# Kernel optimization log

Measured on AMD Instinct MI355X. Metric: run time of the kernel, lower is better.

The kernel has to match this reference:

```python
import jax, jax.numpy as jnp
import numpy as np

K_NODES = 4096
SEQ_L = 32
D_MODEL = 128
D_FF = 512
N_EDGES = 65536
LN_EPS = 1e-5
NEG_SLOPE = 0.2  # PyG GATConv default leaky_relu slope


def setup_inputs() -> dict:
    key = jax.random.key(0)
    ks = jax.random.split(key, 12)
    s = 0.02
    D, F = D_MODEL, D_FF
    return {
        "x": jax.random.normal(ks[0], (1, K_NODES, SEQ_L, D), jnp.float32),
        "edge_index": jax.random.randint(ks[1], (1, 2, N_EDGES), 0, K_NODES, dtype=jnp.int64),
        # temporal TransformerEncoderLayer params (norm_first, 1 head, gelu)
        "ln1_g": jnp.ones((D,), jnp.float32), "ln1_b": jnp.zeros((D,), jnp.float32),
        "qkv_w": jax.random.normal(ks[2], (3 * D, D), jnp.float32) * s,
        "qkv_b": jnp.zeros((3 * D,), jnp.float32),
        "out_w": jax.random.normal(ks[3], (D, D), jnp.float32) * s,
        "out_b": jnp.zeros((D,), jnp.float32),
        "ln2_g": jnp.ones((D,), jnp.float32), "ln2_b": jnp.zeros((D,), jnp.float32),
        "ff1_w": jax.random.normal(ks[4], (F, D), jnp.float32) * s,
        "ff1_b": jnp.zeros((F,), jnp.float32),
        "ff2_w": jax.random.normal(ks[5], (D, F), jnp.float32) * s,
        "ff2_b": jnp.zeros((D,), jnp.float32),
        # GATConv params (heads=1, concat -> out dim D)
        "gat_w": jax.random.normal(ks[6], (D, D), jnp.float32) * s,
        "att_src": jax.random.normal(ks[7], (D,), jnp.float32) * s,
        "att_dst": jax.random.normal(ks[8], (D,), jnp.float32) * s,
        "gat_b": jnp.zeros((D,), jnp.float32),
    }


def _ln(x, g, b):
    m = x.mean(-1, keepdims=True)
    v = ((x - m) ** 2).mean(-1, keepdims=True)
    return (x - m) * jax.lax.rsqrt(v + LN_EPS) * g + b


def _temporal(x, ln1_g, ln1_b, qkv_w, qkv_b, out_w, out_b, ln2_g, ln2_b,
              ff1_w, ff1_b, ff2_w, ff2_b):
    # x: [N, L, D]; pre-norm single-head self-attention + GELU FFN
    D = x.shape[-1]
    h = _ln(x, ln1_g, ln1_b)
    qkv = h @ qkv_w.T + qkv_b
    q, k, v = jnp.split(qkv, 3, axis=-1)
    scores = jnp.einsum('nqd,nkd->nqk', q, k) / jnp.sqrt(jnp.asarray(D, x.dtype))
    a = jax.nn.softmax(scores, axis=-1)
    attn = jnp.einsum('nqk,nkd->nqd', a, v) @ out_w.T + out_b
    x = x + attn
    h = _ln(x, ln2_g, ln2_b)
    ff = jax.nn.gelu(h @ ff1_w.T + ff1_b, approximate=False) @ ff2_w.T + ff2_b
    return x + ff


def _gat(x0, src, dst, gat_w, att_src, att_dst, gat_b):
    # x0: [K, L, D]; vectorized over L (replaces the per-timestep python loop)
    K = x0.shape[0]
    h = jnp.einsum('kld,ed->kle', x0, gat_w)              # [K, L, D]
    a_s = jnp.einsum('kld,d->kl', h, att_src)             # [K, L]
    a_d = jnp.einsum('kld,d->kl', h, att_dst)
    e = jax.nn.leaky_relu(a_s[src] + a_d[dst], NEG_SLOPE)  # [E', L]
    m = jax.ops.segment_max(e, dst, num_segments=K)
    ex = jnp.exp(e - m[dst])
    denom = jax.ops.segment_sum(ex, dst, num_segments=K)
    alpha = ex / (denom[dst] + 1e-16)
    out = jax.ops.segment_sum(h[src] * alpha[..., None], dst, num_segments=K)
    return out + gat_b


def reference(x, edge_index, ln1_g, ln1_b, qkv_w, qkv_b, out_w, out_b,
              ln2_g, ln2_b, ff1_w, ff1_b, ff2_w, ff2_b,
              gat_w, att_src, att_dst, gat_b):
    B, K, L, D = x.shape
    xt = _temporal(x.reshape(B * K, L, D), ln1_g, ln1_b, qkv_w, qkv_b,
                   out_w, out_b, ln2_g, ln2_b, ff1_w, ff1_b, ff2_w, ff2_b)
    xt = xt.reshape(B, K, L, D)
    # GATConv adds self-loops by default
    loops = jnp.arange(K, dtype=edge_index.dtype)
    src = jnp.concatenate([edge_index[0, 0], loops])
    dst = jnp.concatenate([edge_index[0, 1], loops])
    out0 = _gat(xt[0], src, dst, gat_w, att_src, att_dst, gat_b)  # [K, L, D]
    res = jnp.zeros_like(x).at[0].set(out0)
    return res
```

## Files before the change

### kernel.cpp

```cpp
#include <hip/hip_runtime.h>

#define KNODES 4096
#define SEQL 32
#define DM 128
#define DFF 512
#define NEDGE 65536
#define NETOT (NEDGE + KNODES)

typedef float f32x4 __attribute__((ext_vector_type(4)));
typedef short s16x8 __attribute__((ext_vector_type(8)));
typedef short s16x4 __attribute__((ext_vector_type(4)));

#define MFMA16(a, b, c) __builtin_amdgcn_mfma_f32_16x16x32_bf16(a, b, c, 0, 0, 0)

#define F_OUT 96
#define F_FF1 128
#define F_FF2 256
#define F_GAT 384
#define NFRAG 416

__device__ __forceinline__ short f2bf(float f) {
  union { float f; unsigned u; } v; v.f = f;
  unsigned r = (v.u + 0x7FFFu + ((v.u >> 16) & 1u)) >> 16;
  return (short)r;
}

__device__ __forceinline__ float gelu_exact(float v) {
  return 0.5f * v * (1.f + erff(v * 0.70710678118654752440f));
}

__device__ __forceinline__ void ln_to_bf16(const float* XF, short* AB,
                                           const float* __restrict__ g,
                                           const float* __restrict__ b,
                                           int r, int cb) {
  const float* xr = XF + r * 132 + cb;
  float v[8]; float s = 0.f, ss = 0.f;
#pragma unroll
  for (int i = 0; i < 8; ++i) { v[i] = xr[i]; s += v[i]; ss += v[i] * v[i]; }
  s += __shfl_xor(s, 1); ss += __shfl_xor(ss, 1);
  s += __shfl_xor(s, 2); ss += __shfl_xor(ss, 2);
  s += __shfl_xor(s, 4); ss += __shfl_xor(ss, 4);
  s += __shfl_xor(s, 8); ss += __shfl_xor(ss, 8);
  const float mean = s * (1.f / 128.f);
  const float var = ss * (1.f / 128.f) - mean * mean;
  const float rs = rsqrtf(var + 1e-5f);
  const float* gp = g + cb; const float* bp = b + cb;
  short o[8];
#pragma unroll
  for (int i = 0; i < 8; ++i) o[i] = f2bf((v[i] - mean) * rs * gp[i] + bp[i]);
  *(s16x8*)(AB + r * 136 + cb) = *(s16x8*)o;
}

__global__ __launch_bounds__(512, 4) void temporal_kernel(
    const float* __restrict__ x,
    const float* __restrict__ ln1_g, const float* __restrict__ ln1_b,
    const short* __restrict__ wpk, const float* __restrict__ qkv_b,
    const float* __restrict__ out_b,
    const float* __restrict__ ln2_g, const float* __restrict__ ln2_b,
    const float* __restrict__ ff1_b, const float* __restrict__ ff2_b,
    const float* __restrict__ att_src, const float* __restrict__ att_dst,
    short* __restrict__ h_out, float* __restrict__ as_out, float* __restrict__ ad_out) {
  __shared__ __align__(16) char smem[53248];
  float* XF = (float*)smem;
  short* AB = (short*)(smem + 16896);
  float* Sf = (float*)(smem + 16896);
  short* Pb = (short*)(smem + 21504);
  short* Qb = (short*)(smem + 25600);
  short* Kb = (short*)(smem + 34304);
  short* Fb = (short*)(smem + 25600);
  short* Vt = (short*)(smem + 43008);

  const int t = threadIdx.x;
  const int w = t >> 6;
  const int lane = t & 63;
  const int q = lane >> 4, c = lane & 15;
  const int n = blockIdx.x;
  const int r16 = t >> 4, cb8 = (t & 15) * 8;

#define WPK(f) ((const s16x8*)(wpk + (size_t)(f) * 512 + lane * 8))

  s16x8 bwq[3][4];
#pragma unroll
  for (int ii = 0; ii < 3; ++ii)
#pragma unroll
    for (int kt = 0; kt < 4; ++kt)
      bwq[ii][kt] = *WPK((w * 3 + ii) * 4 + kt);

  {
#pragma unroll
    for (int i = t; i < 1024; i += 512) {
      const int row = i >> 5, c4i = i & 31;
      *(float4*)(XF + row * 132 + c4i * 4) =
          *(const float4*)(x + (size_t)n * (SEQL * DM) + i * 4);
    }
  }
  __syncthreads();

  ln_to_bf16(XF, AB, ln1_g, ln1_b, r16, cb8);
  __syncthreads();

  {
    s16x8 a[2][4];
#pragma unroll
    for (int mt = 0; mt < 2; ++mt)
#pragma unroll
      for (int kt = 0; kt < 4; ++kt)
        a[mt][kt] = *(const s16x8*)(AB + (mt * 16 + c) * 136 + kt * 32 + q * 8);
#pragma unroll
    for (int ii = 0; ii < 3; ++ii) {
      const int n0 = (w * 3 + ii) * 16;
      f32x4 acc0 = {0.f, 0.f, 0.f, 0.f}, acc1 = {0.f, 0.f, 0.f, 0.f};
#pragma unroll
      for (int kt = 0; kt < 4; ++kt) {
        acc0 = MFMA16(a[0][kt], bwq[ii][kt], acc0);
        acc1 = MFMA16(a[1][kt], bwq[ii][kt], acc1);
      }
      const float bias = qkv_b[n0 + c];
      if (n0 < 128) {
#pragma unroll
        for (int i = 0; i < 4; ++i) {
          Qb[(q * 4 + i) * 136 + n0 + c] = f2bf(acc0[i] + bias);
          Qb[(16 + q * 4 + i) * 136 + n0 + c] = f2bf(acc1[i] + bias);
        }
      } else if (n0 < 256) {
        const int cc = n0 - 128 + c;
#pragma unroll
        for (int i = 0; i < 4; ++i) {
          Kb[(q * 4 + i) * 136 + cc] = f2bf(acc0[i] + bias);
          Kb[(16 + q * 4 + i) * 136 + cc] = f2bf(acc1[i] + bias);
        }
      } else {
        const int d = n0 - 256 + c;
        s16x4 p0, p1;
#pragma unroll
        for (int i = 0; i < 4; ++i) { p0[i] = f2bf(acc0[i] + bias); p1[i] = f2bf(acc1[i] + bias); }
        *(s16x4*)(Vt + d * 40 + q * 4) = p0;
        *(s16x4*)(Vt + d * 40 + 16 + q * 4) = p1;
      }
    }
  }
  __syncthreads();

  if (w < 4) {
    const int mt = w & 1, nt = w >> 1;
    s16x8 aq[4], bk[4];
#pragma unroll
    for (int kt = 0; kt < 4; ++kt) {
      aq[kt] = *(const s16x8*)(Qb + (mt * 16 + c) * 136 + kt * 32 + q * 8);
      bk[kt] = *(const s16x8*)(Kb + (nt * 16 + c) * 136 + kt * 32 + q * 8);
    }
    f32x4 acc = {0.f, 0.f, 0.f, 0.f};
#pragma unroll
    for (int kt = 0; kt < 4; ++kt) acc = MFMA16(aq[kt], bk[kt], acc);
#pragma unroll
    for (int i = 0; i < 4; ++i)
      Sf[(mt * 16 + q * 4 + i) * 36 + nt * 16 + c] = acc[i] * 0.08838834764831845f;
  }
  __syncthreads();

  if (t < 256) {
    const int r8 = t >> 3, c4 = (t & 7) * 4;
    float4 sv = *(const float4*)(Sf + r8 * 36 + c4);
    float mx = fmaxf(fmaxf(sv.x, sv.y), fmaxf(sv.z, sv.w));
    mx = fmaxf(mx, __shfl_xor(mx, 1));
    mx = fmaxf(mx, __shfl_xor(mx, 2));
    mx = fmaxf(mx, __shfl_xor(mx, 4));
    float e0 = expf(sv.x - mx), e1 = expf(sv.y - mx), e2 = expf(sv.z - mx), e3 = expf(sv.w - mx);
    float sum = e0 + e1 + e2 + e3;
    sum += __shfl_xor(sum, 1);
    sum += __shfl_xor(sum, 2);
    sum += __shfl_xor(sum, 4);
    const float inv = 1.f / sum;
    s16x4 pw; pw[0] = f2bf(e0 * inv); pw[1] = f2bf(e1 * inv); pw[2] = f2bf(e2 * inv); pw[3] = f2bf(e3 * inv);
    *(s16x4*)(Pb + r8 * 40 + c4) = pw;
  }
  __syncthreads();

  s16x8 bwp[4];
  {
#pragma unroll
    for (int kt = 0; kt < 4; ++kt) bwp[kt] = *WPK(F_OUT + w * 4 + kt);
    s16x8 ap0 = *(const s16x8*)(Pb + c * 40 + q * 8);
    s16x8 ap1 = *(const s16x8*)(Pb + (16 + c) * 40 + q * 8);
    const int d0 = w * 16;
    s16x8 bv = *(const s16x8*)(Vt + (d0 + c) * 40 + q * 8);
    f32x4 acc0 = {0.f, 0.f, 0.f, 0.f}, acc1 = {0.f, 0.f, 0.f, 0.f};
    acc0 = MFMA16(ap0, bv, acc0);
    acc1 = MFMA16(ap1, bv, acc1);
#pragma unroll
    for (int i = 0; i < 4; ++i) {
      Qb[(q * 4 + i) * 136 + d0 + c] = f2bf(acc0[i]);
      Qb[(16 + q * 4 + i) * 136 + d0 + c] = f2bf(acc1[i]);
    }
  }
  __syncthreads();

  {
    s16x8 aa[2][4];
#pragma unroll
    for (int mt = 0; mt < 2; ++mt)
#pragma unroll
      for (int kt = 0; kt < 4; ++kt)
        aa[mt][kt] = *(const s16x8*)(Qb + (mt * 16 + c) * 136 + kt * 32 + q * 8);
    const int n0 = w * 16;
    f32x4 acc0 = {0.f, 0.f, 0.f, 0.f}, acc1 = {0.f, 0.f, 0.f, 0.f};
#pragma unroll
    for (int kt = 0; kt < 4; ++kt) {
      acc0 = MFMA16(aa[0][kt], bwp[kt], acc0);
      acc1 = MFMA16(aa[1][kt], bwp[kt], acc1);
    }
    const float bias = out_b[n0 + c];
#pragma unroll
    for (int i = 0; i < 4; ++i) {
      XF[(q * 4 + i) * 132 + n0 + c] += acc0[i] + bias;
      XF[(16 + q * 4 + i) * 132 + n0 + c] += acc1[i] + bias;
    }
  }
  __syncthreads();

  ln_to_bf16(XF, AB, ln2_g, ln2_b, r16, cb8);
  __syncthreads();

  {
    s16x8 af[2][4];
#pragma unroll
    for (int mt = 0; mt < 2; ++mt)
#pragma unroll
      for (int kt = 0; kt < 4; ++kt)
        af[mt][kt] = *(const s16x8*)(AB + (mt * 16 + c) * 136 + kt * 32 + q * 8);
    f32x4 facc0 = {0.f, 0.f, 0.f, 0.f}, facc1 = {0.f, 0.f, 0.f, 0.f};

    for (int ch = 0; ch < 2; ++ch) {
      s16x8 bw1[2][4], bw2[8];
#pragma unroll
      for (int ii = 0; ii < 2; ++ii)
#pragma unroll
        for (int kt = 0; kt < 4; ++kt)
          bw1[ii][kt] = *WPK(F_FF1 + (ch * 16 + w * 2 + ii) * 4 + kt);
#pragma unroll
      for (int kt = 0; kt < 8; ++kt)
        bw2[kt] = *WPK(F_FF2 + w * 16 + ch * 8 + kt);

#pragma unroll
      for (int ii = 0; ii < 2; ++ii) {
        const int ntl = w * 2 + ii;
        const int n0g = ch * 256 + ntl * 16;
        f32x4 acc0 = {0.f, 0.f, 0.f, 0.f}, acc1 = {0.f, 0.f, 0.f, 0.f};
#pragma unroll
        for (int kt = 0; kt < 4; ++kt) {
          acc0 = MFMA16(af[0][kt], bw1[ii][kt], acc0);
          acc1 = MFMA16(af[1][kt], bw1[ii][kt], acc1);
        }
        const float bias = ff1_b[n0g + c];
#pragma unroll
        for (int i = 0; i < 4; ++i) {
          Fb[(q * 4 + i) * 264 + ntl * 16 + c] = f2bf(gelu_exact(acc0[i] + bias));
          Fb[(16 + q * 4 + i) * 264 + ntl * 16 + c] = f2bf(gelu_exact(acc1[i] + bias));
        }
      }
      __syncthreads();
#pragma unroll
      for (int kt = 0; kt < 8; ++kt) {
        s16x8 a0 = *(const s16x8*)(Fb + c * 264 + kt * 32 + q * 8);
        s16x8 a1 = *(const s16x8*)(Fb + (16 + c) * 264 + kt * 32 + q * 8);
        facc0 = MFMA16(a0, bw2[kt], facc0);
        facc1 = MFMA16(a1, bw2[kt], facc1);
      }
      __syncthreads();
    }
    {
      const int n0 = w * 16;
      const float bias = ff2_b[n0 + c];
#pragma unroll
      for (int i = 0; i < 4; ++i) {
        const int r0 = q * 4 + i, r1 = 16 + q * 4 + i;
        AB[r0 * 136 + n0 + c] = f2bf(XF[r0 * 132 + n0 + c] + facc0[i] + bias);
        AB[r1 * 136 + n0 + c] = f2bf(XF[r1 * 132 + n0 + c] + facc1[i] + bias);
      }
    }
  }
  s16x8 bwg[4];
#pragma unroll
  for (int kt = 0; kt < 4; ++kt) bwg[kt] = *WPK(F_GAT + w * 4 + kt);
  __syncthreads();

  {
    s16x8 ag[2][4];
#pragma unroll
    for (int mt = 0; mt < 2; ++mt)
#pragma unroll
      for (int kt = 0; kt < 4; ++kt)
        ag[mt][kt] = *(const s16x8*)(AB + (mt * 16 + c) * 136 + kt * 32 + q * 8);
    const int n0 = w * 16;
    f32x4 acc0 = {0.f, 0.f, 0.f, 0.f}, acc1 = {0.f, 0.f, 0.f, 0.f};
#pragma unroll
    for (int kt = 0; kt < 4; ++kt) {
      acc0 = MFMA16(ag[0][kt], bwg[kt], acc0);
      acc1 = MFMA16(ag[1][kt], bwg[kt], acc1);
    }
#pragma unroll
    for (int i = 0; i < 4; ++i) {
      const int r0 = q * 4 + i, r1 = 16 + q * 4 + i;
      XF[r0 * 132 + n0 + c] = acc0[i];
      XF[r1 * 132 + n0 + c] = acc1[i];
    }
  }
  __syncthreads();

  {
    const int row = t >> 4;
    const float* xr = XF + row * 132 + cb8;
    short o[8];
#pragma unroll
    for (int i = 0; i < 8; ++i) o[i] = f2bf(xr[i]);
    *(s16x8*)(h_out + ((size_t)n * SEQL + row) * DM + cb8) = *(s16x8*)o;
  }

  if (t < 64) {
    const int row = t & 31;
    const float* vec = (t < 32) ? att_src : att_dst;
    const float* hr = XF + row * 132;
    float s = 0.f;
#pragma unroll
    for (int d = 0; d < DM; d += 4)
      s += hr[d] * vec[d] + hr[d + 1] * vec[d + 1] + hr[d + 2] * vec[d + 2] + hr[d + 3] * vec[d + 3];
    if (t < 32) as_out[n * SEQL + row] = s;
    else        ad_out[n * SEQL + row] = s;
  }
}

__global__ void cvt_weights(const float* __restrict__ qkv_w, const float* __restrict__ out_w,
                            const float* __restrict__ ff1_w, const float* __restrict__ ff2_w,
                            const float* __restrict__ gat_w, short* __restrict__ wpk) {
  const int u = blockIdx.x * 256 + threadIdx.x;
  if (u >= NFRAG * 64) return;
  const int f = u >> 6, lane = u & 63;
  const int q = lane >> 4, c = lane & 15;
  const float* src; int row, kt, ld;
  if (f < F_OUT)       { src = qkv_w; ld = 128; int g = f;         row = (g >> 2) * 16 + c; kt = g & 3; }
  else if (f < F_FF1)  { src = out_w; ld = 128; int g = f - F_OUT; row = (g >> 2) * 16 + c; kt = g & 3; }
  else if (f < F_FF2)  { src = ff1_w; ld = 128; int g = f - F_FF1; row = (g >> 2) * 16 + c; kt = g & 3; }
  else if (f < F_GAT)  { src = ff2_w; ld = 512; int g = f - F_FF2; row = (g >> 4) * 16 + c; kt = g & 15; }
  else                 { src = gat_w; ld = 128; int g = f - F_GAT; row = (g >> 2) * 16 + c; kt = g & 3; }
  const float* p = src + row * ld + kt * 32 + q * 8;
  const float4 v0 = *(const float4*)p;
  const float4 v1 = *(const float4*)(p + 4);
  s16x8 o;
  o[0] = f2bf(v0.x); o[1] = f2bf(v0.y); o[2] = f2bf(v0.z); o[3] = f2bf(v0.w);
  o[4] = f2bf(v1.x); o[5] = f2bf(v1.y); o[6] = f2bf(v1.z); o[7] = f2bf(v1.w);
  *(s16x8*)(wpk + (size_t)f * 512 + lane * 8) = o;
}

__global__ void zero_counts(int* counts) {
  int i = blockIdx.x * 256 + threadIdx.x;
  if (i < KNODES) counts[i] = 0;
}

__global__ void hist_kernel(const int* __restrict__ ei, int* counts) {
  int i = blockIdx.x * 256 + threadIdx.x;
  if (i < NETOT) {
    int dst = (i < NEDGE) ? ei[NEDGE + i] : (i - NEDGE);
    atomicAdd(&counts[dst], 1);
  }
}

__global__ void scan_kernel(const int* __restrict__ counts, int* offs, int* cursor) {
  __shared__ int tmp[1024];
  const int t = threadIdx.x;
  const int base = t * 4;
  int c0 = counts[base], c1 = counts[base + 1], c2 = counts[base + 2], c3 = counts[base + 3];
  const int s = c0 + c1 + c2 + c3;
  tmp[t] = s;
  __syncthreads();
  for (int off = 1; off < 1024; off <<= 1) {
    int v = (t >= off) ? tmp[t - off] : 0;
    __syncthreads();
    tmp[t] += v;
    __syncthreads();
  }
  int o = tmp[t] - s;
  offs[base] = o; cursor[base] = o; o += c0;
  offs[base + 1] = o; cursor[base + 1] = o; o += c1;
  offs[base + 2] = o; cursor[base + 2] = o; o += c2;
  offs[base + 3] = o; cursor[base + 3] = o; o += c3;
  if (t == 1023) offs[KNODES] = o;
}

__global__ void scatter_kernel(const int* __restrict__ ei, int* cursor, int* __restrict__ csr) {
  int i = blockIdx.x * 256 + threadIdx.x;
  if (i < NETOT) {
    int src, dst;
    if (i < NEDGE) { src = ei[i]; dst = ei[NEDGE + i]; }
    else           { src = dst = i - NEDGE; }
    int pos = atomicAdd(&cursor[dst], 1);
    csr[pos] = src;
  }
}

#define ECH 32
__global__ __launch_bounds__(256) void gat_aggregate(
    const short* __restrict__ h, const float* __restrict__ as_g, const float* __restrict__ ad_g,
    const int* __restrict__ offs, const int* __restrict__ csr,
    const float* __restrict__ gat_b, float* __restrict__ out) {
  __shared__ float ad_s[16];
  __shared__ float ew[ECH * 17];
  __shared__ int   srcs[ECH];
  __shared__ float dred[16 * 33];
  __shared__ float invd[16];

  const int t = threadIdx.x;
  const int n = blockIdx.x;
  const int l0 = blockIdx.y * 16;
  if (t < 16) ad_s[t] = ad_g[n * SEQL + l0 + t];
  __syncthreads();
  const int beg = offs[n], end = offs[n + 1];

  const int s = t >> 3, lq = t & 7;
  float dpart0 = 0.f, dpart1 = 0.f;

  const int r = t >> 4;
  const int cl = (t & 15) * 8;
  const size_t roff = (size_t)(l0 + r) * DM + cl;
  float acc[8];
#pragma unroll
  for (int j = 0; j < 8; ++j) acc[j] = 0.f;

  for (int cb = beg; cb < end; cb += ECH) {
    const int cnt = min(ECH, end - cb);
    if (s < cnt) {
      const int src = csr[cb + s];
      if (lq == 0) srcs[s] = src;
      const float2 av = *(const float2*)(as_g + src * SEQL + l0 + lq * 2);
      float v0 = av.x + ad_s[lq * 2];
      v0 = v0 > 0.f ? v0 : 0.2f * v0;
      const float e0 = __expf(v0);
      float v1 = av.y + ad_s[lq * 2 + 1];
      v1 = v1 > 0.f ? v1 : 0.2f * v1;
      const float e1 = __expf(v1);
      ew[s * 17 + lq * 2] = e0;
      ew[s * 17 + lq * 2 + 1] = e1;
      dpart0 += e0; dpart1 += e1;
    }
    __syncthreads();

    s16x8 p0, p1, p2, p3;
#define GLOAD(dst, idx)                                                        \
    if ((idx) < cnt)                                                           \
      dst = *(const s16x8*)(h + (size_t)srcs[idx] * (SEQL * DM) + roff)
    GLOAD(p0, 0); GLOAD(p1, 1); GLOAD(p2, 2); GLOAD(p3, 3);

#define CONSUME(p, idx)                                                        \
    if ((idx) < cnt) {                                                         \
      const float wgt = ew[(idx) * 17 + r];                                    \
      const unsigned* pu = (const unsigned*)&(p);                              \
      _Pragma("unroll")                                                        \
      for (int j = 0; j < 4; ++j) {                                           \
        acc[2 * j]     += wgt * __uint_as_float(pu[j] << 16);                  \
        acc[2 * j + 1] += wgt * __uint_as_float(pu[j] & 0xFFFF0000u);          \
      }                                                                        \
    }

    for (int ss = 0; ss < cnt; ss += 4) {
      s16x8 n0, n1, n2, n3;
      GLOAD(n0, ss + 4); GLOAD(n1, ss + 5); GLOAD(n2, ss + 6); GLOAD(n3, ss + 7);
      CONSUME(p0, ss);
      CONSUME(p1, ss + 1);
      CONSUME(p2, ss + 2);
      CONSUME(p3, ss + 3);
      p0 = n0; p1 = n1; p2 = n2; p3 = n3;
    }
#undef GLOAD
#undef CONSUME
    __syncthreads();
  }

  dred[(lq * 2) * 33 + s] = dpart0;
  dred[(lq * 2 + 1) * 33 + s] = dpart1;
  __syncthreads();
  if (t < 16) {
    float sum = 0.f;
#pragma unroll
    for (int s2 = 0; s2 < 32; ++s2) sum += dred[t * 33 + s2];
    invd[t] = 1.f / (sum + 1e-16f);
  }
  __syncthreads();

  const float iv = invd[r];
  float4 b0 = *(const float4*)(gat_b + cl);
  float4 b1 = *(const float4*)(gat_b + cl + 4);
  float4 o0, o1;
  o0.x = acc[0] * iv + b0.x; o0.y = acc[1] * iv + b0.y;
  o0.z = acc[2] * iv + b0.z; o0.w = acc[3] * iv + b0.w;
  o1.x = acc[4] * iv + b1.x; o1.y = acc[5] * iv + b1.y;
  o1.z = acc[6] * iv + b1.z; o1.w = acc[7] * iv + b1.w;
  float* op = out + (size_t)n * (SEQL * DM) + (l0 + r) * DM + cl;
  *(float4*)op = o0;
  *(float4*)(op + 4) = o1;
}

extern "C" void kernel_launch(void* const* d_in, const int* in_sizes, int n_in,
                              void* d_out, int out_size, void* d_ws, size_t ws_size,
                              hipStream_t stream) {
  const float* x       = (const float*)d_in[0];
  const int* ei        = (const int*)d_in[1];
  const float* ln1_g   = (const float*)d_in[2];
  const float* ln1_b   = (const float*)d_in[3];
  const float* qkv_w   = (const float*)d_in[4];
  const float* qkv_b   = (const float*)d_in[5];
  const float* out_w   = (const float*)d_in[6];
  const float* out_b   = (const float*)d_in[7];
  const float* ln2_g   = (const float*)d_in[8];
  const float* ln2_b   = (const float*)d_in[9];
  const float* ff1_w   = (const float*)d_in[10];
  const float* ff1_b   = (const float*)d_in[11];
  const float* ff2_w   = (const float*)d_in[12];
  const float* ff2_b   = (const float*)d_in[13];
  const float* gat_w   = (const float*)d_in[14];
  const float* att_src = (const float*)d_in[15];
  const float* att_dst = (const float*)d_in[16];
  const float* gat_b   = (const float*)d_in[17];
  float* out = (float*)d_out;

  short* h    = (short*)d_ws;
  float* as_g = (float*)(h + (size_t)KNODES * SEQL * DM);
  float* ad_g = as_g + KNODES * SEQL;
  int* counts = (int*)(ad_g + KNODES * SEQL);
  int* offs   = counts + KNODES;
  int* cursor = offs + KNODES + 1;
  int* csr    = cursor + KNODES;
  size_t wofs = (size_t)((char*)(csr + NETOT) - (char*)d_ws);
  wofs = (wofs + 1023) & ~(size_t)1023;
  short* wpk = (short*)((char*)d_ws + wofs);

  cvt_weights<<<(NFRAG * 64 + 255) / 256, 256, 0, stream>>>(qkv_w, out_w, ff1_w, ff2_w, gat_w, wpk);
  zero_counts<<<(KNODES + 255) / 256, 256, 0, stream>>>(counts);
  hist_kernel<<<(NETOT + 255) / 256, 256, 0, stream>>>(ei, counts);
  scan_kernel<<<1, 1024, 0, stream>>>(counts, offs, cursor);
  scatter_kernel<<<(NETOT + 255) / 256, 256, 0, stream>>>(ei, cursor, csr);
  temporal_kernel<<<KNODES, 512, 0, stream>>>(
      x, ln1_g, ln1_b, wpk, qkv_b, out_b, ln2_g, ln2_b,
      ff1_b, ff2_b, att_src, att_dst, h, as_g, ad_g);
  gat_aggregate<<<dim3(KNODES, 2), 256, 0, stream>>>(h, as_g, ad_g, offs, csr, gat_b, out);
}
```

Measured before the change: 357.5 us.

## Restructure GAT aggregation into single-wave blocks of four sequence rows

The GAT aggregation kernel now uses 64-thread single-wavefront blocks, each covering 4 sequence positions, with an (8, KNODES) grid so blocks of the same node run adjacently. The denominator reduction moves from shared memory plus barriers to wave shuffles, the edge chunk shrinks to 16, and output is written with nontemporal stores. The aim is to cut block-level synchronisation and shared-memory reduction overhead and improve L2 locality across the row groups. The cost is that each block now re-reads the CSR list and attention logits, so those reads happen four times as often.

```diff
diff --git a/kernel.cpp b/kernel.cpp
--- a/kernel.cpp
+++ b/kernel.cpp
@@ -397,30 +397,27 @@
   }
 }
 
-#define ECH 32
-__global__ __launch_bounds__(256) void gat_aggregate(
+#define ECH 16
+__global__ __launch_bounds__(64) void gat_aggregate(
     const short* __restrict__ h, const float* __restrict__ as_g, const float* __restrict__ ad_g,
     const int* __restrict__ offs, const int* __restrict__ csr,
     const float* __restrict__ gat_b, float* __restrict__ out) {
-  __shared__ float ad_s[16];
-  __shared__ float ew[ECH * 17];
+  __shared__ float ew[ECH * 5];
   __shared__ int   srcs[ECH];
-  __shared__ float dred[16 * 33];
-  __shared__ float invd[16];
 
   const int t = threadIdx.x;
-  const int n = blockIdx.x;
-  const int l0 = blockIdx.y * 16;
-  if (t < 16) ad_s[t] = ad_g[n * SEQL + l0 + t];
-  __syncthreads();
+  const int lg = blockIdx.x;
+  const int n = blockIdx.y;
+  const int l0 = lg * 4;
+
+  const int s = t >> 2, lr = t & 3;
+  const int r = t >> 4, cl = (t & 15) * 8;
+
+  const float adv = ad_g[n * SEQL + l0 + lr];
   const int beg = offs[n], end = offs[n + 1];
-
-  const int s = t >> 3, lq = t & 7;
-  float dpart0 = 0.f, dpart1 = 0.f;
-
-  const int r = t >> 4;
-  const int cl = (t & 15) * 8;
   const size_t roff = (size_t)(l0 + r) * DM + cl;
+
+  float dpart = 0.f;
   float acc[8];
 #pragma unroll
   for (int j = 0; j < 8; ++j) acc[j] = 0.f;
@@ -429,17 +426,12 @@
     const int cnt = min(ECH, end - cb);
     if (s < cnt) {
       const int src = csr[cb + s];
-      if (lq == 0) srcs[s] = src;
-      const float2 av = *(const float2*)(as_g + src * SEQL + l0 + lq * 2);
-      float v0 = av.x + ad_s[lq * 2];
-      v0 = v0 > 0.f ? v0 : 0.2f * v0;
-      const float e0 = __expf(v0);
-      float v1 = av.y + ad_s[lq * 2 + 1];
-      v1 = v1 > 0.f ? v1 : 0.2f * v1;
-      const float e1 = __expf(v1);
-      ew[s * 17 + lq * 2] = e0;
-      ew[s * 17 + lq * 2 + 1] = e1;
-      dpart0 += e0; dpart1 += e1;
+      if (lr == 0) srcs[s] = src;
+      float v = as_g[src * SEQL + l0 + lr] + adv;
+      v = v > 0.f ? v : 0.2f * v;
+      const float e = __expf(v);
+      ew[s * 5 + lr] = e;
+      dpart += e;
     }
     __syncthreads();
 
@@ -451,7 +443,7 @@
 
 #define CONSUME(p, idx)                                                        \
     if ((idx) < cnt) {                                                         \
-      const float wgt = ew[(idx) * 17 + r];                                    \
+      const float wgt = ew[(idx) * 5 + r];                                     \
       const unsigned* pu = (const unsigned*)&(p);                              \
       _Pragma("unroll")                                                        \
       for (int j = 0; j < 4; ++j) {                                           \
@@ -474,28 +466,22 @@
     __syncthreads();
   }
 
-  dred[(lq * 2) * 33 + s] = dpart0;
-  dred[(lq * 2 + 1) * 33 + s] = dpart1;
-  __syncthreads();
-  if (t < 16) {
-    float sum = 0.f;
-#pragma unroll
-    for (int s2 = 0; s2 < 32; ++s2) sum += dred[t * 33 + s2];
-    invd[t] = 1.f / (sum + 1e-16f);
-  }
-  __syncthreads();
-
-  const float iv = invd[r];
-  float4 b0 = *(const float4*)(gat_b + cl);
-  float4 b1 = *(const float4*)(gat_b + cl + 4);
-  float4 o0, o1;
-  o0.x = acc[0] * iv + b0.x; o0.y = acc[1] * iv + b0.y;
-  o0.z = acc[2] * iv + b0.z; o0.w = acc[3] * iv + b0.w;
-  o1.x = acc[4] * iv + b1.x; o1.y = acc[5] * iv + b1.y;
-  o1.z = acc[6] * iv + b1.z; o1.w = acc[7] * iv + b1.w;
+  dpart += __shfl_xor(dpart, 4);
+  dpart += __shfl_xor(dpart, 8);
+  dpart += __shfl_xor(dpart, 16);
+  dpart += __shfl_xor(dpart, 32);
+  const float iv = 1.f / (__shfl(dpart, r) + 1e-16f);
+
+  const float4 b0 = *(const float4*)(gat_b + cl);
+  const float4 b1 = *(const float4*)(gat_b + cl + 4);
+  f32x4 o0, o1;
+  o0[0] = acc[0] * iv + b0.x; o0[1] = acc[1] * iv + b0.y;
+  o0[2] = acc[2] * iv + b0.z; o0[3] = acc[3] * iv + b0.w;
+  o1[0] = acc[4] * iv + b1.x; o1[1] = acc[5] * iv + b1.y;
+  o1[2] = acc[6] * iv + b1.z; o1[3] = acc[7] * iv + b1.w;
   float* op = out + (size_t)n * (SEQL * DM) + (l0 + r) * DM + cl;
-  *(float4*)op = o0;
-  *(float4*)(op + 4) = o1;
+  __builtin_nontemporal_store(o0, (f32x4*)op);
+  __builtin_nontemporal_store(o1, (f32x4*)(op + 4));
 }
 
 extern "C" void kernel_launch(void* const* d_in, const int* in_sizes, int n_in,
@@ -540,5 +526,5 @@
   temporal_kernel<<<KNODES, 512, 0, stream>>>(
       x, ln1_g, ln1_b, wpk, qkv_b, out_b, ln2_g, ln2_b,
       ff1_b, ff2_b, att_src, att_dst, h, as_g, ad_g);
-  gat_aggregate<<<dim3(KNODES, 2), 256, 0, stream>>>(h, as_g, ad_g, offs, csr, gat_b, out);
-}
+  gat_aggregate<<<dim3(8, KNODES), 64, 0, stream>>>(h, as_g, ad_g, offs, csr, gat_b, out);
+}
```

New measurement: 326.2 us. 8.8% less time.
